# Kernel tuning notes

Hardware: AMD Instinct MI355X
Metric: run time of the kernel (lower is better)

## Reference

```python
import jax, jax.numpy as jnp
import numpy as np

B, S, E, H, V, L = 64, 128, 512, 1024, 32000, 1


def setup_inputs() -> dict:
    key = jax.random.key(0)
    ks = jax.random.split(key, 12)
    def rn(k, shape, scale=0.02):
        return jax.random.normal(k, shape, dtype=jnp.float32) * scale
    return dict(
        emb=rn(ks[0], (B, E), 1.0),
        hidden=rn(ks[1], (L, B, H), 1.0),
        encoder_outputs=rn(ks[2], (S, B, H), 1.0),
        z=rn(ks[3], (B, H), 1.0),
        # Attn('concat'): W_a [H, 2H], bias, scoring vector v [H]
        Wa=rn(ks[4], (H, 2 * H)), ba=jnp.zeros((H,), jnp.float32),
        v=rn(ks[5], (H,)),
        # CustomGRUCell: input/hidden/context/latent-z to 3*H gate projections
        Wx=rn(ks[6], (3 * H, E)), bx=jnp.zeros((3 * H,), jnp.float32),
        Wh=rn(ks[7], (3 * H, H)), bh=jnp.zeros((3 * H,), jnp.float32),
        Wc=rn(ks[8], (3 * H, H)), bc=jnp.zeros((3 * H,), jnp.float32),
        Wz=rn(ks[9], (3 * H, H)), bz=jnp.zeros((3 * H,), jnp.float32),
        # rnn2out: Linear(H, V)
        Wout=rn(ks[10], (V, H)), bout=jnp.zeros((V,), jnp.float32),
    )


def reference(emb, hidden, encoder_outputs, z, Wa, ba, v,
              Wx, bx, Wh, bh, Wc, bc, Wz, bz, Wout, bout):
    h_last = hidden[-1]                                              # [B,H]
    # Bahdanau 'concat' attention: score = v . tanh(Wa @ [h; enc] + ba)
    hS = jnp.broadcast_to(h_last[None], encoder_outputs.shape)       # [S,B,H]
    energy = jnp.tanh(jnp.concatenate([hS, encoder_outputs], axis=-1) @ Wa.T + ba)  # [S,B,H]
    scores = jnp.einsum('sbh,h->bs', energy, v)                      # [B,S]
    attn_weights = jax.nn.softmax(scores, axis=-1)[:, None, :]       # [B,1,S]
    enc_bt = jnp.transpose(encoder_outputs, (1, 0, 2))               # [B,S,H]
    context = jnp.einsum('bos,bsh->bh', attn_weights, enc_bt)        # [B,H]
    # Custom GRU cell: gates get extra context and latent-z additive terms
    gx = emb @ Wx.T + bx                                             # [B,3H]
    gh = h_last @ Wh.T + bh
    gc = context @ Wc.T + bc
    gz = z @ Wz.T + bz
    xr, xu, xn = jnp.split(gx + gc + gz, 3, axis=-1)
    hr, hu, hn = jnp.split(gh, 3, axis=-1)
    r = jax.nn.sigmoid(xr + hr)                                      # reset gate
    u = jax.nn.sigmoid(xu + hu)                                      # update gate
    n = jnp.tanh(xn + r * hn)                                        # candidate
    h_new = (1.0 - u) * n + u * h_last                               # [B,H]
    out = h_new @ Wout.T + bout                                      # [B,V] logits
    return out, h_new[None], attn_weights
```

## Files before the change

kernel.cpp:

```cpp
#include <hip/hip_runtime.h>
#include <hip/hip_bf16.h>
#include <math.h>

#define B_  64
#define S_  128
#define E_  512
#define H_  1024
#define V_  32000
#define H3_ 3072
#define NT_ 16
#define NGC 14

typedef __attribute__((ext_vector_type(8))) short bf16x8;
typedef __attribute__((ext_vector_type(4))) float f32x4;

__device__ __forceinline__ unsigned short f2b(float f) {
    unsigned int u = __builtin_bit_cast(unsigned int, f);
    u = (u + 0x7fffu + ((u >> 16) & 1u)) >> 16;
    return (unsigned short)u;
}

__device__ __forceinline__ void tile_acc(const float* __restrict__ A, int lda,
                                         const float* __restrict__ Wrow0, int ldw,
                                         int kspan, int t, float c[4][4],
                                         float (*As)[64], float (*Ws)[64]) {
    const int tx = t & 15, ty = t >> 4;
    const int lm = t >> 2;
    const int lk = (t & 3) * 4;
    float4 av = *(const float4*)&A[lm * lda + lk];
    float4 wv = *(const float4*)&Wrow0[(size_t)lm * ldw + lk];
    for (int k0 = 0; k0 < kspan; k0 += 16) {
        As[lk + 0][lm] = av.x; As[lk + 1][lm] = av.y;
        As[lk + 2][lm] = av.z; As[lk + 3][lm] = av.w;
        Ws[lk + 0][lm] = wv.x; Ws[lk + 1][lm] = wv.y;
        Ws[lk + 2][lm] = wv.z; Ws[lk + 3][lm] = wv.w;
        __syncthreads();
        if (k0 + 16 < kspan) {
            av = *(const float4*)&A[lm * lda + k0 + 16 + lk];
            wv = *(const float4*)&Wrow0[(size_t)lm * ldw + k0 + 16 + lk];
        }
        #pragma unroll
        for (int k = 0; k < 16; ++k) {
            float4 a = *(const float4*)&As[k][ty * 4];
            float4 w = *(const float4*)&Ws[k][tx * 4];
            c[0][0] += a.x * w.x; c[0][1] += a.x * w.y; c[0][2] += a.x * w.z; c[0][3] += a.x * w.w;
            c[1][0] += a.y * w.x; c[1][1] += a.y * w.y; c[1][2] += a.y * w.z; c[1][3] += a.y * w.w;
            c[2][0] += a.z * w.x; c[2][1] += a.z * w.y; c[2][2] += a.z * w.z; c[2][3] += a.z * w.w;
            c[3][0] += a.w * w.x; c[3][1] += a.w * w.y; c[3][2] += a.w * w.z; c[3][3] += a.w * w.w;
        }
        __syncthreads();
    }
}

__device__ __forceinline__ void hproj_body(int bx, int by, const float* __restrict__ h,
                                           const float* __restrict__ Wa, float* __restrict__ hpp,
                                           int t, float (*As)[64], float (*Ws)[64]) {
    const int n0 = bx * 64;
    const int kb = by * 128;
    const int tx = t & 15, ty = t >> 4;
    float c[4][4];
    #pragma unroll
    for (int i = 0; i < 4; ++i)
        #pragma unroll
        for (int j = 0; j < 4; ++j) c[i][j] = 0.f;
    tile_acc(&h[kb], H_, &Wa[(size_t)n0 * (2 * H_) + kb], 2 * H_, 128, t, c, As, Ws);
    float* dst = hpp + (size_t)by * B_ * H_;
    #pragma unroll
    for (int i = 0; i < 4; ++i) {
        const int m = ty * 4 + i;
        #pragma unroll
        for (int j = 0; j < 4; ++j)
            dst[m * H_ + n0 + tx * 4 + j] = c[i][j];
    }
}

__global__ __launch_bounds__(256) void prologue(
    const float* __restrict__ enc, const float* __restrict__ Wa,
    const float* __restrict__ h, unsigned short* __restrict__ encb,
    unsigned short* __restrict__ wa2b, float* __restrict__ hpp) {
    __shared__ float As[16][64];
    __shared__ float Ws[16][64];
    const int bid = blockIdx.x;
    const int t = threadIdx.x;
    if (bid < 4096) {
        const size_t i8 = ((size_t)bid * 256 + t) * 8;
        float4 a = *(const float4*)&enc[i8];
        float4 b = *(const float4*)&enc[i8 + 4];
        unsigned short o[8] = { f2b(a.x), f2b(a.y), f2b(a.z), f2b(a.w),
                                f2b(b.x), f2b(b.y), f2b(b.z), f2b(b.w) };
        *(uint4*)&encb[i8] = *(uint4*)o;
    } else if (bid < 4608) {
        const int id = (bid - 4096) * 256 + t;
        const int n = id >> 7;
        const int kk = (id & 127) * 8;
        const float* src = &Wa[(size_t)n * (2 * H_) + H_ + kk];
        float4 a = *(const float4*)src;
        float4 b = *(const float4*)(src + 4);
        unsigned short o[8] = { f2b(a.x), f2b(a.y), f2b(a.z), f2b(a.w),
                                f2b(b.x), f2b(b.y), f2b(b.z), f2b(b.w) };
        *(uint4*)&wa2b[(size_t)n * H_ + kk] = *(uint4*)o;
    } else {
        const int id = bid - 4608;
        hproj_body(id & 15, id >> 4, h, Wa, hpp, t, As, Ws);
    }
}

__global__ void hproj_splitk(const float* __restrict__ h, const float* __restrict__ Wa,
                             float* __restrict__ hpp) {
    __shared__ float As[16][64];
    __shared__ float Ws[16][64];
    hproj_body(blockIdx.x, blockIdx.y, h, Wa, hpp, threadIdx.x, As, Ws);
}

__global__ void reduce_hproj(const float* __restrict__ hpp, const float* __restrict__ ba,
                             float* __restrict__ hproj) {
    const int idx = blockIdx.x * 256 + threadIdx.x;
    const int hh = idx & 1023;
    float s = ba[hh];
    #pragma unroll
    for (int c = 0; c < 8; ++c) s += hpp[(size_t)c * B_ * H_ + idx];
    hproj[idx] = s;
}

__global__ __launch_bounds__(256) void energy_mfma(
    const unsigned short* __restrict__ Ab, const unsigned short* __restrict__ Bb,
    const float* __restrict__ hproj, const float* __restrict__ v,
    float* __restrict__ partials) {
    __shared__ unsigned short As[128 * 64];
    __shared__ unsigned short Bs[128 * 64];
    const int nb = blockIdx.x;
    const int mb = blockIdx.y;
    const int m0 = mb * 128, n0 = nb * 128;
    const int t = threadIdx.x;
    const int lane = t & 63, w = t >> 6;
    const int wr = w >> 1, wc = w & 1;

    f32x4 acc[4][4];
    #pragma unroll
    for (int i = 0; i < 4; ++i)
        #pragma unroll
        for (int j = 0; j < 4; ++j) acc[i][j] = (f32x4){0.f, 0.f, 0.f, 0.f};

    for (int k0 = 0; k0 < H_; k0 += 64) {
        #pragma unroll
        for (int r = 0; r < 4; ++r) {
            const int c = r * 256 + t;
            const int row = c >> 3, slot = c & 7;
            const int sw = slot ^ (row & 7);
            uint4 da = *(const uint4*)&Ab[(size_t)(m0 + row) * H_ + k0 + slot * 8];
            *(uint4*)((char*)As + row * 128 + sw * 16) = da;
            uint4 db = *(const uint4*)&Bb[(size_t)(n0 + row) * H_ + k0 + slot * 8];
            *(uint4*)((char*)Bs + row * 128 + sw * 16) = db;
        }
        __syncthreads();
        #pragma unroll
        for (int kk = 0; kk < 2; ++kk) {
            bf16x8 a[4], b[4];
            #pragma unroll
            for (int i = 0; i < 4; ++i) {
                const int row = wr * 64 + i * 16 + (lane & 15);
                const int sw = (kk * 4 + (lane >> 4)) ^ (row & 7);
                a[i] = *(const bf16x8*)((const char*)As + row * 128 + sw * 16);
            }
            #pragma unroll
            for (int j = 0; j < 4; ++j) {
                const int row = wc * 64 + j * 16 + (lane & 15);
                const int sw = (kk * 4 + (lane >> 4)) ^ (row & 7);
                b[j] = *(const bf16x8*)((const char*)Bs + row * 128 + sw * 16);
            }
            #pragma unroll
            for (int i = 0; i < 4; ++i)
                #pragma unroll
                for (int j = 0; j < 4; ++j)
                    acc[i][j] = __builtin_amdgcn_mfma_f32_16x16x32_bf16(a[i], b[j], acc[i][j], 0, 0, 0);
        }
        __syncthreads();
    }

    float vj[4];
    #pragma unroll
    for (int j = 0; j < 4; ++j) vj[j] = v[n0 + wc * 64 + j * 16 + (lane & 15)];

    const int s = mb * 2 + wr;
    #pragma unroll
    for (int i = 0; i < 4; ++i) {
        #pragma unroll
        for (int q = 0; q < 4; ++q) {
            const int b = i * 16 + (lane >> 4) * 4 + q;
            float sum = 0.f;
            #pragma unroll
            for (int j = 0; j < 4; ++j) {
                const int n = n0 + wc * 64 + j * 16 + (lane & 15);
                sum += vj[j] * tanhf(acc[i][j][q] + hproj[b * H_ + n]);
            }
            sum += __shfl_xor(sum, 1);
            sum += __shfl_xor(sum, 2);
            sum += __shfl_xor(sum, 4);
            sum += __shfl_xor(sum, 8);
            if ((lane & 15) == 0)
                partials[((size_t)b * S_ + s) * NT_ + nb * 2 + wc] = sum;
        }
    }
}

__global__ void energy_scores(const float* __restrict__ enc, const float* __restrict__ Wa,
                              const float* __restrict__ hproj, const float* __restrict__ v,
                              float* __restrict__ partials) {
    __shared__ float As[16][64];
    __shared__ float Ws[16][64];
    __shared__ float red[64][16];
    const int nt = blockIdx.x;
    const int s  = blockIdx.y;
    const int n0 = nt * 64;
    const float* Arow = enc + (size_t)s * (B_ * H_);
    const int t  = threadIdx.x;
    const int tx = t & 15, ty = t >> 4;
    float c[4][4];
    #pragma unroll
    for (int i = 0; i < 4; ++i)
        #pragma unroll
        for (int j = 0; j < 4; ++j) c[i][j] = 0.f;
    tile_acc(Arow, H_, &Wa[(size_t)n0 * (2 * H_) + H_], 2 * H_, H_, t, c, As, Ws);
    #pragma unroll
    for (int i = 0; i < 4; ++i) {
        const int b = ty * 4 + i;
        float part = 0.f;
        #pragma unroll
        for (int j = 0; j < 4; ++j) {
            const int h = n0 + tx * 4 + j;
            part += v[h] * tanhf(c[i][j] + hproj[b * H_ + h]);
        }
        red[b][tx] = part;
    }
    __syncthreads();
    if (t < 64) {
        float sum = 0.f;
        #pragma unroll
        for (int x = 0; x < 16; ++x) sum += red[t][x];
        partials[((size_t)t * S_ + s) * NT_ + nt] = sum;
    }
}

__global__ __launch_bounds__(256) void softmax_ctx(
    const float* __restrict__ spart, const float* __restrict__ enc,
    float* __restrict__ attn, float* __restrict__ ctx) {
    __shared__ float red[128];
    __shared__ float aw[128];
    const int b = blockIdx.y;
    const int t = threadIdx.x;
    if (t < 128) {
        float sc = 0.f;
        #pragma unroll
        for (int nt = 0; nt < NT_; ++nt) sc += spart[((size_t)b * S_ + t) * NT_ + nt];
        aw[t] = sc;
        red[t] = sc;
    }
    __syncthreads();
    for (int o = 64; o > 0; o >>= 1) {
        if (t < o) red[t] = fmaxf(red[t], red[t + o]);
        __syncthreads();
    }
    const float mx = red[0];
    __syncthreads();
    if (t < 128) { aw[t] = expf(aw[t] - mx); red[t] = aw[t]; }
    __syncthreads();
    for (int o = 64; o > 0; o >>= 1) {
        if (t < o) red[t] += red[t + o];
        __syncthreads();
    }
    const float inv = 1.f / red[0];
    if (t < 128) {
        aw[t] *= inv;
        if (blockIdx.x == 0) attn[b * S_ + t] = aw[t];
    }
    __syncthreads();
    const int h = blockIdx.x * 256 + t;
    float acc = 0.f;
    for (int s = 0; s < S_; ++s)
        acc += aw[s] * enc[((size_t)s * B_ + b) * H_ + h];
    ctx[b * H_ + h] = acc;
}

__global__ void gates_splitk(const float* __restrict__ emb, const float* __restrict__ z,
                             const float* __restrict__ ctx, const float* __restrict__ h,
                             const float* __restrict__ Wx, const float* __restrict__ Wz,
                             const float* __restrict__ Wc, const float* __restrict__ Wh,
                             float* __restrict__ P) {
    __shared__ float As[16][64];
    __shared__ float Ws[16][64];
    const int n0 = blockIdx.x * 64;
    const int yc = blockIdx.y;
    const int t  = threadIdx.x;
    const int tx = t & 15, ty = t >> 4;
    const float* A; const float* W; int lda, kb;
    if (yc < 2)       { A = emb; W = Wx; lda = E_; kb = yc * 256; }
    else if (yc < 6)  { A = z;   W = Wz; lda = H_; kb = (yc - 2) * 256; }
    else if (yc < 10) { A = ctx; W = Wc; lda = H_; kb = (yc - 6) * 256; }
    else              { A = h;   W = Wh; lda = H_; kb = (yc - 10) * 256; }
    float c[4][4];
    #pragma unroll
    for (int i = 0; i < 4; ++i)
        #pragma unroll
        for (int j = 0; j < 4; ++j) c[i][j] = 0.f;
    tile_acc(&A[kb], lda, &W[(size_t)n0 * lda + kb], lda, 256, t, c, As, Ws);
    float* dst = P + (size_t)yc * B_ * H3_;
    #pragma unroll
    for (int i = 0; i < 4; ++i) {
        const int m = ty * 4 + i;
        #pragma unroll
        for (int j = 0; j < 4; ++j)
            dst[m * H3_ + n0 + tx * 4 + j] = c[i][j];
    }
}

__global__ void gru_k(const float* __restrict__ P, const float* __restrict__ hlast,
                      const float* __restrict__ bx, const float* __restrict__ bz,
                      const float* __restrict__ bc, const float* __restrict__ bh,
                      float* __restrict__ hnew, unsigned short* __restrict__ hnewb) {
    const int idx = blockIdx.x * 256 + threadIdx.x;
    const int b = idx >> 10, h = idx & 1023;
    float x[3], hg[3];
    #pragma unroll
    for (int g = 0; g < 3; ++g) {
        const int col = g * H_ + h;
        float sx = bx[col] + bz[col] + bc[col];
        #pragma unroll
        for (int c = 0; c < 10; ++c) sx += P[((size_t)c * B_ + b) * H3_ + col];
        float sh = bh[col];
        #pragma unroll
        for (int c = 10; c < 14; ++c) sh += P[((size_t)c * B_ + b) * H3_ + col];
        x[g] = sx; hg[g] = sh;
    }
    const float r = 1.f / (1.f + expf(-(x[0] + hg[0])));
    const float u = 1.f / (1.f + expf(-(x[1] + hg[1])));
    const float n = tanhf(x[2] + r * hg[2]);
    const float val = (1.f - u) * n + u * hlast[idx];
    hnew[idx] = val;
    if (hnewb) hnewb[idx] = f2b(val);
}

__global__ __launch_bounds__(256) void wout_mfma(
    const unsigned short* __restrict__ Ab, const float* __restrict__ W,
    const float* __restrict__ bias, float* __restrict__ C) {
    __shared__ unsigned short As[64 * 64];
    __shared__ unsigned short Bs[64 * 64];
    const int n0 = blockIdx.x * 64;
    const int t = threadIdx.x;
    const int lane = t & 63, w = t >> 6;
    const int wr = w >> 1, wc = w & 1;

    f32x4 acc[2][2];
    #pragma unroll
    for (int i = 0; i < 2; ++i)
        #pragma unroll
        for (int j = 0; j < 2; ++j) acc[i][j] = (f32x4){0.f, 0.f, 0.f, 0.f};

    for (int k0 = 0; k0 < H_; k0 += 64) {
        #pragma unroll
        for (int r = 0; r < 2; ++r) {
            const int c = r * 256 + t;
            const int row = c >> 3, slot = c & 7;
            const int sw = slot ^ (row & 7);
            uint4 da = *(const uint4*)&Ab[(size_t)row * H_ + k0 + slot * 8];
            *(uint4*)((char*)As + row * 128 + sw * 16) = da;
        }
        #pragma unroll
        for (int r = 0; r < 4; ++r) {
            const int c = r * 256 + t;
            const int row = c >> 4, q4 = c & 15;
            const float4 wv = *(const float4*)&W[(size_t)(n0 + row) * H_ + k0 + q4 * 4];
            uint2 pk;
            pk.x = (unsigned int)f2b(wv.x) | ((unsigned int)f2b(wv.y) << 16);
            pk.y = (unsigned int)f2b(wv.z) | ((unsigned int)f2b(wv.w) << 16);
            const int slot = q4 >> 1, half = q4 & 1;
            const int sw = slot ^ (row & 7);
            *(uint2*)((char*)Bs + row * 128 + sw * 16 + half * 8) = pk;
        }
        __syncthreads();
        #pragma unroll
        for (int kk = 0; kk < 2; ++kk) {
            bf16x8 a[2], b[2];
            #pragma unroll
            for (int i = 0; i < 2; ++i) {
                const int row = wr * 32 + i * 16 + (lane & 15);
                const int sw = (kk * 4 + (lane >> 4)) ^ (row & 7);
                a[i] = *(const bf16x8*)((const char*)As + row * 128 + sw * 16);
            }
            #pragma unroll
            for (int j = 0; j < 2; ++j) {
                const int row = wc * 32 + j * 16 + (lane & 15);
                const int sw = (kk * 4 + (lane >> 4)) ^ (row & 7);
                b[j] = *(const bf16x8*)((const char*)Bs + row * 128 + sw * 16);
            }
            #pragma unroll
            for (int i = 0; i < 2; ++i)
                #pragma unroll
                for (int j = 0; j < 2; ++j)
                    acc[i][j] = __builtin_amdgcn_mfma_f32_16x16x32_bf16(a[i], b[j], acc[i][j], 0, 0, 0);
        }
        __syncthreads();
    }

    #pragma unroll
    for (int i = 0; i < 2; ++i)
        #pragma unroll
        for (int j = 0; j < 2; ++j) {
            const int n = n0 + wc * 32 + j * 16 + (lane & 15);
            const float bn = bias[n];
            #pragma unroll
            for (int q = 0; q < 4; ++q) {
                const int m = wr * 32 + i * 16 + (lane >> 4) * 4 + q;
                C[(size_t)m * V_ + n] = acc[i][j][q] + bn;
            }
        }
}

__global__ void gemm_nt(const float* __restrict__ A, const float* __restrict__ W,
                        const float* __restrict__ bias, float* __restrict__ C,
                        int N, int K) {
    __shared__ float As[16][64];
    __shared__ float Ws[16][64];
    const int n0 = blockIdx.x * 64;
    const int t  = threadIdx.x;
    const int tx = t & 15, ty = t >> 4;
    float c[4][4];
    #pragma unroll
    for (int i = 0; i < 4; ++i)
        #pragma unroll
        for (int j = 0; j < 4; ++j) c[i][j] = 0.f;
    tile_acc(A, K, &W[(size_t)n0 * K], K, K, t, c, As, Ws);
    #pragma unroll
    for (int i = 0; i < 4; ++i) {
        const int m = ty * 4 + i;
        #pragma unroll
        for (int j = 0; j < 4; ++j) {
            const int n = n0 + tx * 4 + j;
            C[m * N + n] = c[i][j] + bias[n];
        }
    }
}

extern "C" void kernel_launch(void* const* d_in, const int* in_sizes, int n_in,
                              void* d_out, int out_size, void* d_ws, size_t ws_size,
                              hipStream_t stream) {
    const float* emb   = (const float*)d_in[0];
    const float* hid   = (const float*)d_in[1];
    const float* enc   = (const float*)d_in[2];
    const float* z     = (const float*)d_in[3];
    const float* Wa    = (const float*)d_in[4];
    const float* ba    = (const float*)d_in[5];
    const float* v     = (const float*)d_in[6];
    const float* Wx    = (const float*)d_in[7];
    const float* bx    = (const float*)d_in[8];
    const float* Wh    = (const float*)d_in[9];
    const float* bh    = (const float*)d_in[10];
    const float* Wc    = (const float*)d_in[11];
    const float* bc    = (const float*)d_in[12];
    const float* Wz    = (const float*)d_in[13];
    const float* bz    = (const float*)d_in[14];
    const float* Wout  = (const float*)d_in[15];
    const float* bout  = (const float*)d_in[16];

    float* out  = (float*)d_out;
    float* hnew = out + (size_t)B_ * V_;
    float* attn = hnew + (size_t)B_ * H_;

    float* hproj = (float*)d_ws;
    float* spart = hproj + (size_t)B_ * H_;
    float* ctx   = spart + (size_t)B_ * S_ * NT_;
    float* hpp   = ctx + (size_t)B_ * H_;
    float* P     = hpp + (size_t)8 * B_ * H_;
    float* fend  = P + (size_t)NGC * B_ * H3_;
    unsigned short* hnewb = (unsigned short*)fend;
    unsigned short* encb  = hnewb + (size_t)B_ * H_;
    unsigned short* wa2b  = encb + (size_t)S_ * B_ * H_;
    const size_t need = (size_t)((char*)(wa2b + (size_t)H_ * H_) - (char*)d_ws);

    const float* hlast = hid;
    dim3 blk(256);

    const bool fast = (ws_size >= need);
    if (fast) {
        prologue<<<dim3(4736), blk, 0, stream>>>(enc, Wa, hlast, encb, wa2b, hpp);
        reduce_hproj<<<dim3((B_ * H_) / 256), blk, 0, stream>>>(hpp, ba, hproj);
        energy_mfma<<<dim3(H_ / 128, (S_ * B_) / 128), blk, 0, stream>>>(encb, wa2b, hproj, v, spart);
        softmax_ctx<<<dim3(H_ / 256, B_), blk, 0, stream>>>(spart, enc, attn, ctx);
        gates_splitk<<<dim3(H3_ / 64, NGC), blk, 0, stream>>>(emb, z, ctx, hlast,
                                                              Wx, Wz, Wc, Wh, P);
        gru_k<<<dim3((B_ * H_) / 256), blk, 0, stream>>>(P, hlast, bx, bz, bc, bh, hnew, hnewb);
        wout_mfma<<<dim3(V_ / 64), blk, 0, stream>>>(hnewb, Wout, bout, out);
    } else {
        hproj_splitk<<<dim3(H_ / 64, 8), blk, 0, stream>>>(hlast, Wa, hpp);
        reduce_hproj<<<dim3((B_ * H_) / 256), blk, 0, stream>>>(hpp, ba, hproj);
        energy_scores<<<dim3(NT_, S_), blk, 0, stream>>>(enc, Wa, hproj, v, spart);
        softmax_ctx<<<dim3(H_ / 256, B_), blk, 0, stream>>>(spart, enc, attn, ctx);
        gates_splitk<<<dim3(H3_ / 64, NGC), blk, 0, stream>>>(emb, z, ctx, hlast,
                                                              Wx, Wz, Wc, Wh, P);
        gru_k<<<dim3((B_ * H_) / 256), blk, 0, stream>>>(P, hlast, bx, bz, bc, bh, hnew, nullptr);
        gemm_nt<<<dim3(V_ / 64), blk, 0, stream>>>(hnew, Wout, bout, out, V_, H_);
    }
}
```

Before: 129.6 us.

## Fuse encoder bf16 conversion into energy MFMA tile loads

```diff
diff --git a/kernel.cpp b/kernel.cpp
--- a/kernel.cpp
+++ b/kernel.cpp
@@ -75,22 +75,14 @@
 }
 
 __global__ __launch_bounds__(256) void prologue(
-    const float* __restrict__ enc, const float* __restrict__ Wa,
-    const float* __restrict__ h, unsigned short* __restrict__ encb,
+    const float* __restrict__ Wa, const float* __restrict__ h,
     unsigned short* __restrict__ wa2b, float* __restrict__ hpp) {
     __shared__ float As[16][64];
     __shared__ float Ws[16][64];
     const int bid = blockIdx.x;
     const int t = threadIdx.x;
-    if (bid < 4096) {
-        const size_t i8 = ((size_t)bid * 256 + t) * 8;
-        float4 a = *(const float4*)&enc[i8];
-        float4 b = *(const float4*)&enc[i8 + 4];
-        unsigned short o[8] = { f2b(a.x), f2b(a.y), f2b(a.z), f2b(a.w),
-                                f2b(b.x), f2b(b.y), f2b(b.z), f2b(b.w) };
-        *(uint4*)&encb[i8] = *(uint4*)o;
-    } else if (bid < 4608) {
-        const int id = (bid - 4096) * 256 + t;
+    if (bid < 512) {
+        const int id = bid * 256 + t;
         const int n = id >> 7;
         const int kk = (id & 127) * 8;
         const float* src = &Wa[(size_t)n * (2 * H_) + H_ + kk];
@@ -100,7 +92,7 @@
                                 f2b(b.x), f2b(b.y), f2b(b.z), f2b(b.w) };
         *(uint4*)&wa2b[(size_t)n * H_ + kk] = *(uint4*)o;
     } else {
-        const int id = bid - 4608;
+        const int id = bid - 512;
         hproj_body(id & 15, id >> 4, h, Wa, hpp, t, As, Ws);
     }
 }
@@ -123,13 +115,13 @@
 }
 
 __global__ __launch_bounds__(256) void energy_mfma(
-    const unsigned short* __restrict__ Ab, const unsigned short* __restrict__ Bb,
+    const float* __restrict__ enc, const unsigned short* __restrict__ Bb,
     const float* __restrict__ hproj, const float* __restrict__ v,
     float* __restrict__ partials) {
     __shared__ unsigned short As[128 * 64];
     __shared__ unsigned short Bs[128 * 64];
-    const int nb = blockIdx.x;
-    const int mb = blockIdx.y;
+    const int mb = blockIdx.x;
+    const int nb = blockIdx.y;
     const int m0 = mb * 128, n0 = nb * 128;
     const int t = threadIdx.x;
     const int lane = t & 63, w = t >> 6;
@@ -143,12 +135,22 @@
 
     for (int k0 = 0; k0 < H_; k0 += 64) {
         #pragma unroll
+        for (int r = 0; r < 8; ++r) {
+            const int c = r * 256 + t;
+            const int row = c >> 4, q4 = c & 15;
+            const float4 av = *(const float4*)&enc[(size_t)(m0 + row) * H_ + k0 + q4 * 4];
+            uint2 pk;
+            pk.x = (unsigned int)f2b(av.x) | ((unsigned int)f2b(av.y) << 16);
+            pk.y = (unsigned int)f2b(av.z) | ((unsigned int)f2b(av.w) << 16);
+            const int slot = q4 >> 1, half = q4 & 1;
+            const int sw = slot ^ (row & 7);
+            *(uint2*)((char*)As + row * 128 + sw * 16 + half * 8) = pk;
+        }
+        #pragma unroll
         for (int r = 0; r < 4; ++r) {
             const int c = r * 256 + t;
             const int row = c >> 3, slot = c & 7;
             const int sw = slot ^ (row & 7);
-            uint4 da = *(const uint4*)&Ab[(size_t)(m0 + row) * H_ + k0 + slot * 8];
-            *(uint4*)((char*)As + row * 128 + sw * 16) = da;
             uint4 db = *(const uint4*)&Bb[(size_t)(n0 + row) * H_ + k0 + slot * 8];
             *(uint4*)((char*)Bs + row * 128 + sw * 16) = db;
         }
@@ -472,8 +474,7 @@
     float* P     = hpp + (size_t)8 * B_ * H_;
     float* fend  = P + (size_t)NGC * B_ * H3_;
     unsigned short* hnewb = (unsigned short*)fend;
-    unsigned short* encb  = hnewb + (size_t)B_ * H_;
-    unsigned short* wa2b  = encb + (size_t)S_ * B_ * H_;
+    unsigned short* wa2b  = hnewb + (size_t)B_ * H_;
     const size_t need = (size_t)((char*)(wa2b + (size_t)H_ * H_) - (char*)d_ws);
 
     const float* hlast = hid;
@@ -481,9 +482,9 @@
 
     const bool fast = (ws_size >= need);
     if (fast) {
-        prologue<<<dim3(4736), blk, 0, stream>>>(enc, Wa, hlast, encb, wa2b, hpp);
+        prologue<<<dim3(640), blk, 0, stream>>>(Wa, hlast, wa2b, hpp);
         reduce_hproj<<<dim3((B_ * H_) / 256), blk, 0, stream>>>(hpp, ba, hproj);
-        energy_mfma<<<dim3(H_ / 128, (S_ * B_) / 128), blk, 0, stream>>>(encb, wa2b, hproj, v, spart);
+        energy_mfma<<<dim3((S_ * B_) / 128, H_ / 128), blk, 0, stream>>>(enc, wa2b, hproj, v, spart);
         softmax_ctx<<<dim3(H_ / 256, B_), blk, 0, stream>>>(spart, enc, attn, ctx);
         gates_splitk<<<dim3(H3_ / 64, NGC), blk, 0, stream>>>(emb, z, ctx, hlast,
                                                               Wx, Wz, Wc, Wh, P);
```

After: 118.7 us. 8.4% less time.
